# Performance work log

Measured on AMD Instinct MI355X. Metric: run time of the kernel, lower is better.

Reference implementation:

```python
import jax, jax.numpy as jnp
import numpy as np

# init config (matches init_kwargs)
NO_TRANS = False
SPATIAL_SCALE = 0.0625
POOLED = 7
SAMPLES = 2          # sampling_ratio (sample_per_part)
TRANS_STD = 0.1

B, C, H, W = 2, 256, 96, 96
N_ROIS = 512


def setup_inputs() -> dict:
    key = jax.random.key(0)
    k1, k2, k3, k4, k5 = jax.random.split(key, 5)
    bottom_data = jax.random.normal(k1, (B, C, H, W), dtype=jnp.float32)
    img = H / SPATIAL_SCALE  # image-space extent (1536)
    bidx = jax.random.randint(k2, (N_ROIS,), 0, B).astype(jnp.float32)
    xy1 = jax.random.uniform(k3, (N_ROIS, 2), minval=0.0, maxval=0.7 * img)
    wh = jax.random.uniform(k4, (N_ROIS, 2), minval=0.05 * img, maxval=0.3 * img)
    bottom_rois = jnp.concatenate([bidx[:, None], xy1, xy1 + wh], axis=1)  # [N,5]
    bottom_trans = jax.random.normal(k5, (N_ROIS, 2, POOLED, POOLED), dtype=jnp.float32)
    return {"bottom_data": bottom_data, "bottom_rois": bottom_rois, "bottom_trans": bottom_trans}


def _deform_psroi_pool(feat, rois, trans):
    # feat [B,C,H,W], rois [N,5], trans [N,2,P,P] -> out [N,C,P,P]
    Hf, Wf = feat.shape[2], feat.shape[3]
    b = rois[:, 0].astype(jnp.int32)                                    # [N]
    # CUDA kernel rounds roi coords, shifts by -0.5
    x1 = jnp.round(rois[:, 1]) * SPATIAL_SCALE - 0.5
    y1 = jnp.round(rois[:, 2]) * SPATIAL_SCALE - 0.5
    x2 = (jnp.round(rois[:, 3]) + 1.0) * SPATIAL_SCALE - 0.5
    y2 = (jnp.round(rois[:, 4]) + 1.0) * SPATIAL_SCALE - 0.5
    rw = jnp.maximum(x2 - x1, 0.1)
    rh = jnp.maximum(y2 - y1, 0.1)
    bin_w = rw / POOLED
    bin_h = rh / POOLED
    sub_w = bin_w / SAMPLES
    sub_h = bin_h / SAMPLES

    grid = jnp.arange(POOLED, dtype=feat.dtype)
    # part_size == pooled_size and group_size == 1 -> part_h=ph, part_w=pw, class 0
    if NO_TRANS:
        trans_x = jnp.zeros((rois.shape[0], POOLED, POOLED), feat.dtype)
        trans_y = trans_x
    else:
        trans_x = trans[:, 0] * TRANS_STD  # [N,P,P]
        trans_y = trans[:, 1] * TRANS_STD

    # bin start coords per (n, ph, pw)
    wstart = grid[None, None, :] * bin_w[:, None, None] + x1[:, None, None] + trans_x * rw[:, None, None]
    hstart = grid[None, :, None] * bin_h[:, None, None] + y1[:, None, None] + trans_y * rh[:, None, None]

    s = jnp.arange(SAMPLES, dtype=feat.dtype)
    # sample coords [N,P,P,S(ih),S(iw)]
    w = wstart[:, :, :, None, None] + s[None, None, None, None, :] * sub_w[:, None, None, None, None]
    h = hstart[:, :, :, None, None] + s[None, None, None, :, None] * sub_h[:, None, None, None, None]

    valid = (w >= -0.5) & (w <= Wf - 0.5) & (h >= -0.5) & (h <= Hf - 0.5)
    wc = jnp.clip(w, 0.0, Wf - 1.0)
    hc = jnp.clip(h, 0.0, Hf - 1.0)
    x0 = jnp.floor(wc); y0 = jnp.floor(hc)
    dx = wc - x0; dy = hc - y0
    x0i = x0.astype(jnp.int32); y0i = y0.astype(jnp.int32)
    x1i = jnp.ceil(wc).astype(jnp.int32); y1i = jnp.ceil(hc).astype(jnp.int32)

    feat_hwc = jnp.transpose(feat, (0, 2, 3, 1))  # [B,H,W,C]
    bb = b[:, None, None, None, None]

    def gather(yi, xi):
        return feat_hwc[bb, yi, xi]  # [N,P,P,S,S,C]

    w00 = ((1.0 - dx) * (1.0 - dy))[..., None]
    w01 = (dx * (1.0 - dy))[..., None]
    w10 = ((1.0 - dx) * dy)[..., None]
    w11 = (dx * dy)[..., None]
    val = (w00 * gather(y0i, x0i) + w01 * gather(y0i, x1i)
           + w10 * gather(y1i, x0i) + w11 * gather(y1i, x1i))
    val = jnp.where(valid[..., None], val, 0.0)

    ssum = val.sum(axis=(3, 4))                              # [N,P,P,C]
    count = valid.astype(feat.dtype).sum(axis=(3, 4))        # [N,P,P]
    out = jnp.where(count[..., None] > 0, ssum / jnp.maximum(count[..., None], 1.0), 0.0)
    return jnp.transpose(out, (0, 3, 1, 2))                  # [N,C,P,P]


def reference(bottom_data, bottom_rois, bottom_trans):
    return _deform_psroi_pool(bottom_data, bottom_rois, bottom_trans)
```

## Files before the change

### kernel.cpp

```cpp
#include <hip/hip_runtime.h>

#define B_      2
#define C_      256
#define H_      96
#define W_      96
#define P_      7
#define NROIS_  512
#define SCALE_  0.0625f
#define TSTD_   0.1f

#define NGROUP_ 8
#define GC_     (C_ / NGROUP_)

__global__ __launch_bounds__(256) void nchw_to_nhwc(const float* __restrict__ in,
                                                    float* __restrict__ out) {
    __shared__ float tile[32][33];
    const int b  = blockIdx.z;
    const int p0 = blockIdx.x * 32;
    const int c0 = blockIdx.y * 32;
    const int tx = threadIdx.x;
    const int ty = threadIdx.y;
    const float* src = in  + (size_t)b * (C_ * H_ * W_);
    float*       dst = out + (size_t)b * (C_ * H_ * W_);
#pragma unroll
    for (int k = 0; k < 32; k += 8)
        tile[ty + k][tx] = src[(size_t)(c0 + ty + k) * (H_ * W_) + p0 + tx];
    __syncthreads();
#pragma unroll
    for (int k = 0; k < 32; k += 8)
        dst[(size_t)(p0 + ty + k) * C_ + c0 + tx] = tile[tx][ty + k];
}

__global__ __launch_bounds__(256) void dpsroi_pool2(const float* __restrict__ feat,
                                                    const float* __restrict__ rois,
                                                    const float* __restrict__ trans,
                                                    float* __restrict__ out) {
    __shared__ float sout[GC_ * P_ * P_];

    const int blk = blockIdx.x;
    const int g   = blk & (NGROUP_ - 1);
    const int n   = blk >> 3;
    const int tid = threadIdx.x;
    const int cl  = (tid & 7) * 4;
    const int cab = g * GC_ + cl;

    const int   broi = (int)rois[n * 5 + 0];
    const float x1 = rintf(rois[n * 5 + 1]) * SCALE_ - 0.5f;
    const float y1 = rintf(rois[n * 5 + 2]) * SCALE_ - 0.5f;
    const float x2 = (rintf(rois[n * 5 + 3]) + 1.0f) * SCALE_ - 0.5f;
    const float y2 = (rintf(rois[n * 5 + 4]) + 1.0f) * SCALE_ - 0.5f;
    const float rw = fmaxf(x2 - x1, 0.1f);
    const float rh = fmaxf(y2 - y1, 0.1f);
    const float bin_w = rw * (1.0f / 7.0f);
    const float bin_h = rh * (1.0f / 7.0f);
    const float sub_w = bin_w * 0.5f;
    const float sub_h = bin_h * 0.5f;

    const float* fb = feat + (size_t)broi * (H_ * W_ * C_) + cab;

    for (int bin = tid >> 3; bin < P_ * P_; bin += 32) {
        const int pi = bin / P_;
        const int pj = bin - pi * P_;

        const float tx = trans[((n * 2 + 0) * P_ + pi) * P_ + pj] * TSTD_;
        const float ty = trans[((n * 2 + 1) * P_ + pi) * P_ + pj] * TSTD_;
        const float wstart = (float)pj * bin_w + x1 + tx * rw;
        const float hstart = (float)pi * bin_h + y1 + ty * rh;

        float acc0 = 0.f, acc1 = 0.f, acc2 = 0.f, acc3 = 0.f;
        int cnt = 0;
#pragma unroll
        for (int sa = 0; sa < 2; ++sa) {
#pragma unroll
            for (int sb = 0; sb < 2; ++sb) {
                const float w = wstart + (float)sb * sub_w;
                const float h = hstart + (float)sa * sub_h;
                if (w >= -0.5f && w <= (float)W_ - 0.5f &&
                    h >= -0.5f && h <= (float)H_ - 0.5f) {
                    ++cnt;
                    const float wc  = fminf(fmaxf(w, 0.0f), (float)(W_ - 1));
                    const float hc  = fminf(fmaxf(h, 0.0f), (float)(H_ - 1));
                    const float x0f = floorf(wc), y0f = floorf(hc);
                    const float dx  = wc - x0f,   dy  = hc - y0f;
                    const int   x0  = (int)x0f,   y0  = (int)y0f;
                    const int   xp  = (int)ceilf(wc), yp = (int)ceilf(hc);
                    const float w00 = (1.0f - dx) * (1.0f - dy);
                    const float w01 = dx * (1.0f - dy);
                    const float w10 = (1.0f - dx) * dy;
                    const float w11 = dx * dy;

                    const float4 v00 = *(const float4*)(fb + ((size_t)y0 * W_ + x0) * C_);
                    const float4 v01 = *(const float4*)(fb + ((size_t)y0 * W_ + xp) * C_);
                    const float4 v10 = *(const float4*)(fb + ((size_t)yp * W_ + x0) * C_);
                    const float4 v11 = *(const float4*)(fb + ((size_t)yp * W_ + xp) * C_);
                    acc0 += w00 * v00.x + w01 * v01.x + w10 * v10.x + w11 * v11.x;
                    acc1 += w00 * v00.y + w01 * v01.y + w10 * v10.y + w11 * v11.y;
                    acc2 += w00 * v00.z + w01 * v01.z + w10 * v10.z + w11 * v11.z;
                    acc3 += w00 * v00.w + w01 * v01.w + w10 * v10.w + w11 * v11.w;
                }
            }
        }

        const float inv = (cnt > 0) ? (1.0f / (float)cnt) : 0.0f;
        sout[(cl + 0) * (P_ * P_) + bin] = acc0 * inv;
        sout[(cl + 1) * (P_ * P_) + bin] = acc1 * inv;
        sout[(cl + 2) * (P_ * P_) + bin] = acc2 * inv;
        sout[(cl + 3) * (P_ * P_) + bin] = acc3 * inv;
    }

    __syncthreads();
    float* outn = out + ((size_t)n * C_ + g * GC_) * (P_ * P_);
    for (int f = tid; f < GC_ * P_ * P_; f += 256)
        outn[f] = sout[f];
}

extern "C" void kernel_launch(void* const* d_in, const int* in_sizes, int n_in,
                              void* d_out, int out_size, void* d_ws, size_t ws_size,
                              hipStream_t stream) {
    const float* feat  = (const float*)d_in[0];
    const float* rois  = (const float*)d_in[1];
    const float* trans = (const float*)d_in[2];
    float* out = (float*)d_out;

    float* hwc = (float*)d_ws;
    dim3 tb(32, 8);
    dim3 tg((H_ * W_) / 32, C_ / 32, B_);
    nchw_to_nhwc<<<tg, tb, 0, stream>>>(feat, hwc);
    dpsroi_pool2<<<NROIS_ * NGROUP_, 256, 0, stream>>>(hwc, rois, trans, out);
}
```

Baseline: 98.16 us.

## Use channel-group-blocked feature layout and branchless batched bilinear gathers

The transpose kernel now writes features as [B, group, H*W, 32] instead of NHWC, so each 8-channel-group block of the pooling kernel reads from a compact 128-byte-per-pixel slab with better cache locality. The pooling inner loop computes all four sample positions' weights and offsets first, masks invalid samples with zero weights instead of branching, and then issues the 16 float4 loads together for more memory-level parallelism. Nontemporal loads and stores are added to the transpose and the output write. Invalid samples still cause loads of clamped addresses, which adds some wasted traffic.

```diff
diff --git a/kernel.cpp b/kernel.cpp
--- a/kernel.cpp
+++ b/kernel.cpp
@@ -4,6 +4,7 @@
 #define C_      256
 #define H_      96
 #define W_      96
+#define HW_     (H_ * W_)
 #define P_      7
 #define NROIS_  512
 #define SCALE_  0.0625f
@@ -12,26 +13,29 @@
 #define NGROUP_ 8
 #define GC_     (C_ / NGROUP_)
 
-__global__ __launch_bounds__(256) void nchw_to_nhwc(const float* __restrict__ in,
-                                                    float* __restrict__ out) {
+__global__ __launch_bounds__(256) void nchw_to_gp(const float* __restrict__ in,
+                                                  float* __restrict__ out) {
     __shared__ float tile[32][33];
     const int b  = blockIdx.z;
     const int p0 = blockIdx.x * 32;
-    const int c0 = blockIdx.y * 32;
+    const int g  = blockIdx.y;
+    const int c0 = g * 32;
     const int tx = threadIdx.x;
     const int ty = threadIdx.y;
-    const float* src = in  + (size_t)b * (C_ * H_ * W_);
-    float*       dst = out + (size_t)b * (C_ * H_ * W_);
+    const float* src = in  + (size_t)b * (C_ * HW_);
+    float*       dst = out + ((size_t)(b * NGROUP_ + g) * HW_) * GC_;
 #pragma unroll
     for (int k = 0; k < 32; k += 8)
-        tile[ty + k][tx] = src[(size_t)(c0 + ty + k) * (H_ * W_) + p0 + tx];
+        tile[ty + k][tx] =
+            __builtin_nontemporal_load(&src[(size_t)(c0 + ty + k) * HW_ + p0 + tx]);
     __syncthreads();
 #pragma unroll
     for (int k = 0; k < 32; k += 8)
-        dst[(size_t)(p0 + ty + k) * C_ + c0 + tx] = tile[tx][ty + k];
+        __builtin_nontemporal_store(tile[tx][ty + k],
+                                    &dst[(size_t)(p0 + ty + k) * GC_ + tx]);
 }
 
-__global__ __launch_bounds__(256) void dpsroi_pool2(const float* __restrict__ feat,
+__global__ __launch_bounds__(256) void dpsroi_pool3(const float* __restrict__ feat,
                                                     const float* __restrict__ rois,
                                                     const float* __restrict__ trans,
                                                     float* __restrict__ out) {
@@ -42,7 +46,6 @@
     const int n   = blk >> 3;
     const int tid = threadIdx.x;
     const int cl  = (tid & 7) * 4;
-    const int cab = g * GC_ + cl;
 
     const int   broi = (int)rois[n * 5 + 0];
     const float x1 = rintf(rois[n * 5 + 1]) * SCALE_ - 0.5f;
@@ -56,7 +59,7 @@
     const float sub_w = bin_w * 0.5f;
     const float sub_h = bin_h * 0.5f;
 
-    const float* fb = feat + (size_t)broi * (H_ * W_ * C_) + cab;
+    const float* fb = feat + ((size_t)(broi * NGROUP_ + g) * HW_) * GC_ + cl;
 
     for (int bin = tid >> 3; bin < P_ * P_; bin += 32) {
         const int pi = bin / P_;
@@ -67,37 +70,51 @@
         const float wstart = (float)pj * bin_w + x1 + tx * rw;
         const float hstart = (float)pi * bin_h + y1 + ty * rh;
 
+        float w4[4], h4[4];
+#pragma unroll
+        for (int s = 0; s < 4; ++s) {
+            w4[s] = wstart + (float)(s & 1) * sub_w;
+            h4[s] = hstart + (float)(s >> 1) * sub_h;
+        }
+        int   cnt = 0;
+        float wt[4][4];
+        int   ofs[4][4];
+#pragma unroll
+        for (int s = 0; s < 4; ++s) {
+            const float w = w4[s], h = h4[s];
+            const bool valid = (w >= -0.5f) & (w <= (float)W_ - 0.5f) &
+                               (h >= -0.5f) & (h <= (float)H_ - 0.5f);
+            cnt += valid ? 1 : 0;
+            const float vf = valid ? 1.0f : 0.0f;
+            const float wc  = fminf(fmaxf(w, 0.0f), (float)(W_ - 1));
+            const float hc  = fminf(fmaxf(h, 0.0f), (float)(H_ - 1));
+            const float x0f = floorf(wc), y0f = floorf(hc);
+            const float dx  = wc - x0f,   dy  = hc - y0f;
+            const int   x0  = (int)x0f,   y0  = (int)y0f;
+            const int   xp  = (int)ceilf(wc), yp = (int)ceilf(hc);
+            wt[s][0] = vf * (1.0f - dx) * (1.0f - dy);
+            wt[s][1] = vf * dx * (1.0f - dy);
+            wt[s][2] = vf * (1.0f - dx) * dy;
+            wt[s][3] = vf * dx * dy;
+            ofs[s][0] = y0 * W_ + x0;
+            ofs[s][1] = y0 * W_ + xp;
+            ofs[s][2] = yp * W_ + x0;
+            ofs[s][3] = yp * W_ + xp;
+        }
+
         float acc0 = 0.f, acc1 = 0.f, acc2 = 0.f, acc3 = 0.f;
-        int cnt = 0;
 #pragma unroll
-        for (int sa = 0; sa < 2; ++sa) {
+        for (int s = 0; s < 4; ++s) {
+            float4 v[4];
 #pragma unroll
-            for (int sb = 0; sb < 2; ++sb) {
-                const float w = wstart + (float)sb * sub_w;
-                const float h = hstart + (float)sa * sub_h;
-                if (w >= -0.5f && w <= (float)W_ - 0.5f &&
-                    h >= -0.5f && h <= (float)H_ - 0.5f) {
-                    ++cnt;
-                    const float wc  = fminf(fmaxf(w, 0.0f), (float)(W_ - 1));
-                    const float hc  = fminf(fmaxf(h, 0.0f), (float)(H_ - 1));
-                    const float x0f = floorf(wc), y0f = floorf(hc);
-                    const float dx  = wc - x0f,   dy  = hc - y0f;
-                    const int   x0  = (int)x0f,   y0  = (int)y0f;
-                    const int   xp  = (int)ceilf(wc), yp = (int)ceilf(hc);
-                    const float w00 = (1.0f - dx) * (1.0f - dy);
-                    const float w01 = dx * (1.0f - dy);
-                    const float w10 = (1.0f - dx) * dy;
-                    const float w11 = dx * dy;
-
-                    const float4 v00 = *(const float4*)(fb + ((size_t)y0 * W_ + x0) * C_);
-                    const float4 v01 = *(const float4*)(fb + ((size_t)y0 * W_ + xp) * C_);
-                    const float4 v10 = *(const float4*)(fb + ((size_t)yp * W_ + x0) * C_);
-                    const float4 v11 = *(const float4*)(fb + ((size_t)yp * W_ + xp) * C_);
-                    acc0 += w00 * v00.x + w01 * v01.x + w10 * v10.x + w11 * v11.x;
-                    acc1 += w00 * v00.y + w01 * v01.y + w10 * v10.y + w11 * v11.y;
-                    acc2 += w00 * v00.z + w01 * v01.z + w10 * v10.z + w11 * v11.z;
-                    acc3 += w00 * v00.w + w01 * v01.w + w10 * v10.w + w11 * v11.w;
-                }
+            for (int c = 0; c < 4; ++c)
+                v[c] = *(const float4*)(fb + (size_t)ofs[s][c] * GC_);
+#pragma unroll
+            for (int c = 0; c < 4; ++c) {
+                acc0 += wt[s][c] * v[c].x;
+                acc1 += wt[s][c] * v[c].y;
+                acc2 += wt[s][c] * v[c].z;
+                acc3 += wt[s][c] * v[c].w;
             }
         }
 
@@ -111,7 +128,7 @@
     __syncthreads();
     float* outn = out + ((size_t)n * C_ + g * GC_) * (P_ * P_);
     for (int f = tid; f < GC_ * P_ * P_; f += 256)
-        outn[f] = sout[f];
+        __builtin_nontemporal_store(sout[f], &outn[f]);
 }
 
 extern "C" void kernel_launch(void* const* d_in, const int* in_sizes, int n_in,
@@ -122,9 +139,9 @@
     const float* trans = (const float*)d_in[2];
     float* out = (float*)d_out;
 
-    float* hwc = (float*)d_ws;
+    float* gp = (float*)d_ws;
     dim3 tb(32, 8);
-    dim3 tg((H_ * W_) / 32, C_ / 32, B_);
-    nchw_to_nhwc<<<tg, tb, 0, stream>>>(feat, hwc);
-    dpsroi_pool2<<<NROIS_ * NGROUP_, 256, 0, stream>>>(hwc, rois, trans, out);
+    dim3 tg(HW_ / 32, NGROUP_, B_);
+    nchw_to_gp<<<tg, tb, 0, stream>>>(feat, gp);
+    dpsroi_pool3<<<NROIS_ * NGROUP_, 256, 0, stream>>>(gp, rois, trans, out);
 }
```

Measured after the change: 101.6 us. 3.5% more time.
